# Performance work log

Hardware: AMD Instinct MI355X
Metric: run time of the kernel (lower is better)

Reference implementation:

```python
import jax, jax.numpy as jnp
import numpy as np

N = 50000          # num_nodes
D = 32             # latent_dim
E2 = 800000        # undirected edge pairs; E = 2*E2 directed edges
STEP = 1.0         # step_size


def setup_inputs() -> dict:
    key = jax.random.key(0)
    k1, k2, k3, k4 = jax.random.split(key, 4)
    # Build a symmetric edge list so every edge (s,t) has its reverse (t,s).
    rng = np.random.default_rng(0)
    src = rng.integers(0, N, size=E2)
    dst = rng.integers(0, N, size=E2)
    edge_index = jnp.asarray(
        np.stack([np.concatenate([src, dst]), np.concatenate([dst, src])]),
        dtype=jnp.int32)                                   # [2, 2*E2]
    # reverse-edge index: edge e in first half <-> e+E2 in second half
    right_idx = jnp.asarray(
        np.concatenate([np.arange(E2) + E2, np.arange(E2)]), dtype=jnp.int32)
    x = jax.random.normal(k1, (N, D), dtype=jnp.float32)
    sheaf_W = jax.random.normal(k2, (1, 2 * D), dtype=jnp.float32) * 0.1
    lin_W = jax.random.normal(k3, (D, D), dtype=jnp.float32) * 0.1
    lin_b = jax.random.normal(k4, (D,), dtype=jnp.float32) * 0.1
    return {"x": x, "sheaf_W": sheaf_W, "lin_W": lin_W, "lin_b": lin_b,
            "edge_index": edge_index, "right_idx": right_idx}


def reference(x, sheaf_W, lin_W, lin_b, edge_index, right_idx):
    row, col = edge_index[0], edge_index[1]
    # predict_restriction_maps: maps = tanh(W_s [x_row ; x_col])  -> [E, 1]
    xe = jnp.concatenate([x[row], x[col]], axis=1)          # [E, 2D]
    maps = jnp.tanh(xe @ sheaf_W.T)                         # [E, 1]
    # build_laplacian (left_idx is identity)
    non_diag = -(maps * maps[right_idx])                    # [E, 1]
    diag_maps = jax.ops.segment_sum(maps ** 2, row, num_segments=N)  # [N, 1]
    d_si = (diag_maps + 1.0) ** -0.5                        # [N, 1]
    norm_maps = d_si[row] * non_diag * d_si[col]            # [E, 1]
    diag = (d_si * diag_maps * d_si)[:, 0]                  # [N]
    # y = linear(x); sparse Laplacian matmul: L @ y
    y = x @ lin_W.T + lin_b                                 # [N, D]
    Ly = diag[:, None] * y + jax.ops.segment_sum(
        norm_maps * y[col], row, num_segments=N)            # [N, D]
    return x - STEP * Ly
```

## Files before the change

### kernel.cpp

```cpp
#include <hip/hip_runtime.h>

#define D 32
#define GBITS 6
#define GSIZE 64
#define BLK 256
#define PPC 4096
#define IPT 16
#define CAP 2560

typedef unsigned long long ull;

static __device__ __forceinline__ unsigned short f2h(float f) {
    _Float16 h = (_Float16)f;
    return __builtin_bit_cast(unsigned short, h);
}
static __device__ __forceinline__ float h2f(unsigned short u) {
    return (float)__builtin_bit_cast(_Float16, u);
}
static __device__ __forceinline__ float ftanh(float u) {
    u = fminf(fmaxf(u, -15.f), 15.f);
    float e = __expf(2.f * u);
    return (e - 1.f) / (e + 1.f);
}

__global__ void k_pre_hist(const float* __restrict__ x,
                           const float* __restrict__ sheafW,
                           const float* __restrict__ linW,
                           const float* __restrict__ linb,
                           const int* __restrict__ ei,
                           float2* __restrict__ ab,
                           unsigned short* __restrict__ y_h,
                           int* __restrict__ bhist,
                           int N, int E2, int E, int nbN, int nblkH, int NBG) {
    if (blockIdx.x < nbN) {
        __shared__ float sW[D * D];
        __shared__ float sB[D];
        __shared__ float sS[2 * D];
        for (int i = threadIdx.x; i < D * D; i += blockDim.x) sW[i] = linW[i];
        if (threadIdx.x < D) sB[threadIdx.x] = linb[threadIdx.x];
        if (threadIdx.x < 2 * D) sS[threadIdx.x] = sheafW[threadIdx.x];
        __syncthreads();

        int n = blockIdx.x * blockDim.x + threadIdx.x;
        if (n >= N) return;

        float xv[D];
        const float4* xp = reinterpret_cast<const float4*>(x + (size_t)n * D);
#pragma unroll
        for (int i = 0; i < D / 4; ++i) {
            float4 v = xp[i];
            xv[4 * i + 0] = v.x; xv[4 * i + 1] = v.y;
            xv[4 * i + 2] = v.z; xv[4 * i + 3] = v.w;
        }

        float av = 0.f, bv = 0.f;
#pragma unroll
        for (int d = 0; d < D; ++d) { av += xv[d] * sS[d]; bv += xv[d] * sS[D + d]; }
        ab[n] = make_float2(av, bv);

        unsigned short yh[D];
#pragma unroll
        for (int j = 0; j < D; ++j) {
            float s = sB[j];
#pragma unroll
            for (int d = 0; d < D; ++d) s += xv[d] * sW[j * D + d];
            yh[j] = f2h(s);
        }
        uint4* dst = reinterpret_cast<uint4*>(y_h + (size_t)n * D);
        const uint4* src = reinterpret_cast<const uint4*>(yh);
#pragma unroll
        for (int q = 0; q < D / 8; ++q) dst[q] = src[q];
    } else {
        __shared__ int hist[1024];
        int blk = blockIdx.x - nbN;
        for (int i = threadIdx.x; i < NBG; i += BLK) hist[i] = 0;
        __syncthreads();
        int base = blk * PPC;
#pragma unroll
        for (int k = 0; k < IPT; ++k) {
            int i = base + k * BLK + threadIdx.x;
            if (i < E2) {
                int s = ei[i];
                int t = ei[E + i];
                atomicAdd(&hist[s >> GBITS], 1);
                atomicAdd(&hist[t >> GBITS], 1);
            }
        }
        __syncthreads();
        for (int i = threadIdx.x; i < NBG; i += BLK)
            bhist[(size_t)i * nblkH + blk] = hist[i];
    }
}

__global__ void k_scanA(int* __restrict__ data, int* __restrict__ bsum, int M) {
    __shared__ int s[256];
    int t = threadIdx.x;
    int i = blockIdx.x * 256 + t;
    int v = (i < M) ? data[i] : 0;
    s[t] = v;
    __syncthreads();
#pragma unroll
    for (int o = 1; o < 256; o <<= 1) {
        int tmp = (t >= o) ? s[t - o] : 0;
        __syncthreads();
        s[t] += tmp;
        __syncthreads();
    }
    if (i < M) data[i] = s[t] - v;
    if (t == 255) bsum[blockIdx.x] = s[255];
}

__global__ void k_scanB(int* __restrict__ data, int NB) {
    __shared__ int s[1024];
    int t = threadIdx.x;
    int per = (NB + 1023) >> 10;
    int beg = t * per;
    int end_ = min(beg + per, NB);
    int sum = 0;
    for (int i = beg; i < end_; ++i) sum += data[i];
    s[t] = sum;
    __syncthreads();
#pragma unroll
    for (int o = 1; o < 1024; o <<= 1) {
        int tmp = (t >= o) ? s[t - o] : 0;
        __syncthreads();
        s[t] += tmp;
        __syncthreads();
    }
    int run = s[t] - sum;
    for (int i = beg; i < end_; ++i) { int v = data[i]; data[i] = run; run += v; }
}

__global__ void k_scatter(const int* __restrict__ ei,
                          const float2* __restrict__ ab,
                          const int* __restrict__ bhist,
                          const int* __restrict__ bsum,
                          ull* __restrict__ binned,
                          int E2, int E, int nblkH, int NBG) {
    __shared__ int cursor[1024];
    for (int i = threadIdx.x; i < NBG; i += BLK) {
        int idx = i * nblkH + blockIdx.x;
        cursor[i] = bhist[idx] + bsum[idx >> 8];
    }
    __syncthreads();
    int base = blockIdx.x * PPC;
#pragma unroll
    for (int k = 0; k < IPT; ++k) {
        int i = base + k * BLK + threadIdx.x;
        if (i < E2) {
            int s = ei[i];
            int t = ei[E + i];
            float2 as = ab[s], at = ab[t];
            float m  = ftanh(as.x + at.y);
            float mr = ftanh(at.x + as.y);
            ull hm = f2h(m), hmr = f2h(mr);
            int pos = atomicAdd(&cursor[s >> GBITS], 1);
            binned[pos] = ((ull)(unsigned)s << 48) | ((ull)(unsigned)t << 32) | (hm << 16) | hmr;
            int pos2 = atomicAdd(&cursor[t >> GBITS], 1);
            binned[pos2] = ((ull)(unsigned)t << 48) | ((ull)(unsigned)s << 32) | (hmr << 16) | hm;
        }
    }
}

__global__ void k_diag(const ull* __restrict__ binned,
                       const int* __restrict__ bhist,
                       const int* __restrict__ bsum,
                       float* __restrict__ dsi, float* __restrict__ diag2,
                       int* __restrict__ rbase_g, int* __restrict__ rcnt_g,
                       int E, int nblkH, int NBG, int N) {
    __shared__ float rdiag[GSIZE];
    __shared__ int rhist[GSIZE];
    __shared__ int ss[GSIZE];
    __shared__ int sgs[2];
    int g = blockIdx.x, t = threadIdx.x;
    if (t < GSIZE) { rdiag[t] = 0.f; rhist[t] = 0; }
    if (t < 2) {
        int gg = g + t;
        if (gg < NBG) {
            int idx = gg * nblkH;
            sgs[t] = bhist[idx] + bsum[idx >> 8];
        } else sgs[t] = E;
    }
    __syncthreads();
    int gstart = sgs[0], gend = sgs[1];
    for (int k = gstart + t; k < gend; k += BLK) {
        ull it = binned[k];
        int r = (int)(it >> 48) & (GSIZE - 1);
        float m = h2f((unsigned short)((it >> 16) & 0xFFFF));
        atomicAdd(&rdiag[r], m * m);
        atomicAdd(&rhist[r], 1);
    }
    __syncthreads();
    int v = (t < GSIZE) ? rhist[t] : 0;
    if (t < GSIZE) ss[t] = v;
    __syncthreads();
#pragma unroll
    for (int o = 1; o < GSIZE; o <<= 1) {
        int tmp = 0;
        if (t < GSIZE && t >= o) tmp = ss[t - o];
        __syncthreads();
        if (t < GSIZE) ss[t] += tmp;
        __syncthreads();
    }
    int n0 = g << GBITS;
    if (t < GSIZE) {
        int n = n0 + t;
        if (n < N) {
            float dm = rdiag[t];
            float ds = rsqrtf(dm + 1.0f);
            dsi[n] = ds;
            diag2[n] = dm * ds * ds;
            rbase_g[n] = ss[t] - v;
            rcnt_g[n] = v;
        }
    }
}

__global__ __launch_bounds__(512) void k_gather_fused(
        const ull* __restrict__ binned,
        const int* __restrict__ bhist,
        const int* __restrict__ bsum,
        const unsigned short* __restrict__ y_h,
        const float* __restrict__ x,
        const float* __restrict__ dsi,
        const float* __restrict__ diag2,
        const int* __restrict__ rbase_g,
        const int* __restrict__ rcnt_g,
        float* __restrict__ out,
        int E, int nblkH, int NBG, int N) {
    __shared__ unsigned int sortedw[CAP];
    __shared__ int rbase[GSIZE];
    __shared__ int rcnt[GSIZE];
    __shared__ int cur[GSIZE];
    __shared__ float sds[GSIZE];
    __shared__ float sdg[GSIZE];
    __shared__ int sgs[1];
    int g = blockIdx.x, t = threadIdx.x;
    int n0 = g << GBITS;
    if (t < GSIZE) {
        int n = n0 + t;
        if (n < N) {
            sds[t] = dsi[n]; sdg[t] = diag2[n];
            int rb = rbase_g[n];
            rbase[t] = rb; cur[t] = rb; rcnt[t] = rcnt_g[n];
        } else { rbase[t] = 0; cur[t] = 0; rcnt[t] = 0; }
    }
    if (t == 0) {
        int idx = g * nblkH;
        sgs[0] = bhist[idx] + bsum[idx >> 8];
    }
    __syncthreads();
    int gstart = sgs[0];
    int cnt = 0;
    {
        int lastn = min(n0 + GSIZE, N) - 1;
        if (lastn >= n0) cnt = min(rbase[lastn - n0] + rcnt[lastn - n0], CAP);
    }

    for (int k = t; k < cnt; k += 512) {
        ull it = binned[gstart + k];
        int r = (int)(it >> 48) & (GSIZE - 1);
        unsigned int c = (unsigned int)((it >> 32) & 0xFFFF);
        float w = h2f((unsigned short)((it >> 16) & 0xFFFF)) *
                  h2f((unsigned short)(it & 0xFFFF)) * dsi[c];
        int pos = atomicAdd(&cur[r], 1);
        sortedw[pos] = (c << 16) | (unsigned int)f2h(w);
    }
    __syncthreads();

    int hw = t >> 5;
    int lane = t & 31;
    int rows = min(GSIZE, N - n0);
    for (int r = hw; r < rows; r += 16) {
        int beg = rbase[r];
        int end_ = beg + rcnt[r];
        float acc = 0.f;
        int k = beg;
        for (; k + 4 <= end_; k += 4) {
            unsigned int e0 = sortedw[k + 0];
            unsigned int e1 = sortedw[k + 1];
            unsigned int e2 = sortedw[k + 2];
            unsigned int e3 = sortedw[k + 3];
            float v0 = h2f(y_h[(size_t)(e0 >> 16) * D + lane]);
            float v1 = h2f(y_h[(size_t)(e1 >> 16) * D + lane]);
            float v2 = h2f(y_h[(size_t)(e2 >> 16) * D + lane]);
            float v3 = h2f(y_h[(size_t)(e3 >> 16) * D + lane]);
            acc += h2f((unsigned short)(e0 & 0xFFFF)) * v0;
            acc += h2f((unsigned short)(e1 & 0xFFFF)) * v1;
            acc += h2f((unsigned short)(e2 & 0xFFFF)) * v2;
            acc += h2f((unsigned short)(e3 & 0xFFFF)) * v3;
        }
        for (; k < end_; ++k) {
            unsigned int e = sortedw[k];
            acc += h2f((unsigned short)(e & 0xFFFF)) *
                   h2f(y_h[(size_t)(e >> 16) * D + lane]);
        }
        size_t p = (size_t)(n0 + r) * D + lane;
        float yown = h2f(y_h[p]);
        out[p] = x[p] - sdg[r] * yown + sds[r] * acc;
    }
}

extern "C" void kernel_launch(void* const* d_in, const int* in_sizes, int n_in,
                              void* d_out, int out_size, void* d_ws, size_t ws_size,
                              hipStream_t stream) {
    const float* x      = (const float*)d_in[0];
    const float* sheafW = (const float*)d_in[1];
    const float* linW   = (const float*)d_in[2];
    const float* linb   = (const float*)d_in[3];
    const int*   ei     = (const int*)d_in[4];

    int N  = in_sizes[0] / D;
    int E  = in_sizes[4] / 2;
    int E2 = E / 2;

    int NBG   = (N + GSIZE - 1) >> GBITS;
    int nblkH = (E2 + PPC - 1) / PPC;
    int MH    = NBG * nblkH;
    int nblkA = (MH + 255) / 256;

    char* wp = (char*)d_ws;
    ull*    binned = (ull*)wp;    wp += (size_t)E * 8;
    float2* ab     = (float2*)wp; wp += (size_t)N * 8;
    float*  dsi    = (float*)wp;  wp += (size_t)N * 4;
    float*  diag2  = (float*)wp;  wp += (size_t)N * 4;
    unsigned short* y_h = (unsigned short*)wp; wp += (size_t)N * D * 2;
    int*    bhist  = (int*)wp;    wp += (size_t)MH * 4;
    int*    bsumA  = (int*)wp;    wp += (size_t)nblkA * 4;
    int*    rbase_g= (int*)wp;    wp += (size_t)N * 4;
    int*    rcnt_g = (int*)wp;    wp += (size_t)N * 4;

    float* out = (float*)d_out;

    int nbN = (N + BLK - 1) / BLK;

    k_pre_hist<<<nbN + nblkH, BLK, 0, stream>>>(x, sheafW, linW, linb, ei, ab, y_h,
                                                bhist, N, E2, E, nbN, nblkH, NBG);
    k_scanA<<<nblkA, 256, 0, stream>>>(bhist, bsumA, MH);
    k_scanB<<<1, 1024, 0, stream>>>(bsumA, nblkA);
    k_scatter<<<nblkH, BLK, 0, stream>>>(ei, ab, bhist, bsumA, binned, E2, E, nblkH, NBG);
    k_diag<<<NBG, BLK, 0, stream>>>(binned, bhist, bsumA, dsi, diag2, rbase_g, rcnt_g,
                                    E, nblkH, NBG, N);
    k_gather_fused<<<NBG, 512, 0, stream>>>(binned, bhist, bsumA, y_h, x, dsi, diag2,
                                            rbase_g, rcnt_g, out, E, nblkH, NBG, N);
}
```

Measured before the change: 92.14 us.

## Merge scan, scatter, diag and gather into one cooperative persistent kernel

Replaces five separate launches (two scan passes, scatter, diag, gather) with a single cooperative kernel of 512 blocks that uses grid.sync between phases and grid-stride loops over chunks and node groups. Histogram/scatter partition size is halved so more chunks exist, and the scan block width changes to 512. The aim is to remove kernel launch gaps and tail effects between short dependent stages. In exchange, each phase runs on a fixed grid that may underfill or serialize work, grid-wide barriers have their own cost, and the 512-thread blocks with large shared arrays may limit residency.

```diff
diff --git a/kernel.cpp b/kernel.cpp
--- a/kernel.cpp
+++ b/kernel.cpp
@@ -1,11 +1,17 @@
 #include <hip/hip_runtime.h>
+#include <hip/hip_cooperative_groups.h>
+
+namespace cg = cooperative_groups;
 
 #define D 32
 #define GBITS 6
 #define GSIZE 64
-#define BLK 256
-#define PPC 4096
-#define IPT 16
+#define BLKP 256
+#define PPC 2048
+#define IPT_H 8
+#define CBLK 512
+#define IPT_S 4
+#define GRID 512
 #define CAP 2560
 
 typedef unsigned long long ull;
@@ -73,12 +79,12 @@
     } else {
         __shared__ int hist[1024];
         int blk = blockIdx.x - nbN;
-        for (int i = threadIdx.x; i < NBG; i += BLK) hist[i] = 0;
+        for (int i = threadIdx.x; i < NBG; i += BLKP) hist[i] = 0;
         __syncthreads();
         int base = blk * PPC;
 #pragma unroll
-        for (int k = 0; k < IPT; ++k) {
-            int i = base + k * BLK + threadIdx.x;
+        for (int k = 0; k < IPT_H; ++k) {
+            int i = base + k * BLKP + threadIdx.x;
             if (i < E2) {
                 int s = ei[i];
                 int t = ei[E + i];
@@ -87,217 +93,217 @@
             }
         }
         __syncthreads();
-        for (int i = threadIdx.x; i < NBG; i += BLK)
+        for (int i = threadIdx.x; i < NBG; i += BLKP)
             bhist[(size_t)i * nblkH + blk] = hist[i];
     }
 }
 
-__global__ void k_scanA(int* __restrict__ data, int* __restrict__ bsum, int M) {
-    __shared__ int s[256];
-    int t = threadIdx.x;
-    int i = blockIdx.x * 256 + t;
-    int v = (i < M) ? data[i] : 0;
-    s[t] = v;
-    __syncthreads();
-#pragma unroll
-    for (int o = 1; o < 256; o <<= 1) {
-        int tmp = (t >= o) ? s[t - o] : 0;
-        __syncthreads();
-        s[t] += tmp;
-        __syncthreads();
-    }
-    if (i < M) data[i] = s[t] - v;
-    if (t == 255) bsum[blockIdx.x] = s[255];
-}
-
-__global__ void k_scanB(int* __restrict__ data, int NB) {
-    __shared__ int s[1024];
-    int t = threadIdx.x;
-    int per = (NB + 1023) >> 10;
-    int beg = t * per;
-    int end_ = min(beg + per, NB);
-    int sum = 0;
-    for (int i = beg; i < end_; ++i) sum += data[i];
-    s[t] = sum;
-    __syncthreads();
-#pragma unroll
-    for (int o = 1; o < 1024; o <<= 1) {
-        int tmp = (t >= o) ? s[t - o] : 0;
-        __syncthreads();
-        s[t] += tmp;
-        __syncthreads();
-    }
-    int run = s[t] - sum;
-    for (int i = beg; i < end_; ++i) { int v = data[i]; data[i] = run; run += v; }
-}
-
-__global__ void k_scatter(const int* __restrict__ ei,
-                          const float2* __restrict__ ab,
-                          const int* __restrict__ bhist,
-                          const int* __restrict__ bsum,
-                          ull* __restrict__ binned,
-                          int E2, int E, int nblkH, int NBG) {
+__global__ __launch_bounds__(CBLK, 4) void k_coop(
+        const int* __restrict__ ei,
+        const float2* __restrict__ ab,
+        int* __restrict__ bhist,
+        int* __restrict__ bsum,
+        ull* __restrict__ binned,
+        const unsigned short* __restrict__ y_h,
+        const float* __restrict__ x,
+        float* __restrict__ dsi,
+        float* __restrict__ diag2,
+        int* __restrict__ rbase_g,
+        int* __restrict__ rcnt_g,
+        float* __restrict__ out,
+        int E2, int E, int nblkH, int NBG, int N, int MH, int nchA) {
+    cg::grid_group grid = cg::this_grid();
+    int bid = blockIdx.x, t = threadIdx.x;
+
+    __shared__ int s512[CBLK];
     __shared__ int cursor[1024];
-    for (int i = threadIdx.x; i < NBG; i += BLK) {
-        int idx = i * nblkH + blockIdx.x;
-        cursor[i] = bhist[idx] + bsum[idx >> 8];
-    }
-    __syncthreads();
-    int base = blockIdx.x * PPC;
-#pragma unroll
-    for (int k = 0; k < IPT; ++k) {
-        int i = base + k * BLK + threadIdx.x;
-        if (i < E2) {
-            int s = ei[i];
-            int t = ei[E + i];
-            float2 as = ab[s], at = ab[t];
-            float m  = ftanh(as.x + at.y);
-            float mr = ftanh(at.x + as.y);
-            ull hm = f2h(m), hmr = f2h(mr);
-            int pos = atomicAdd(&cursor[s >> GBITS], 1);
-            binned[pos] = ((ull)(unsigned)s << 48) | ((ull)(unsigned)t << 32) | (hm << 16) | hmr;
-            int pos2 = atomicAdd(&cursor[t >> GBITS], 1);
-            binned[pos2] = ((ull)(unsigned)t << 48) | ((ull)(unsigned)s << 32) | (hmr << 16) | hm;
-        }
-    }
-}
-
-__global__ void k_diag(const ull* __restrict__ binned,
-                       const int* __restrict__ bhist,
-                       const int* __restrict__ bsum,
-                       float* __restrict__ dsi, float* __restrict__ diag2,
-                       int* __restrict__ rbase_g, int* __restrict__ rcnt_g,
-                       int E, int nblkH, int NBG, int N) {
+    __shared__ unsigned int sortedw[CAP];
     __shared__ float rdiag[GSIZE];
     __shared__ int rhist[GSIZE];
     __shared__ int ss[GSIZE];
-    __shared__ int sgs[2];
-    int g = blockIdx.x, t = threadIdx.x;
-    if (t < GSIZE) { rdiag[t] = 0.f; rhist[t] = 0; }
-    if (t < 2) {
-        int gg = g + t;
-        if (gg < NBG) {
-            int idx = gg * nblkH;
-            sgs[t] = bhist[idx] + bsum[idx >> 8];
-        } else sgs[t] = E;
-    }
-    __syncthreads();
-    int gstart = sgs[0], gend = sgs[1];
-    for (int k = gstart + t; k < gend; k += BLK) {
-        ull it = binned[k];
-        int r = (int)(it >> 48) & (GSIZE - 1);
-        float m = h2f((unsigned short)((it >> 16) & 0xFFFF));
-        atomicAdd(&rdiag[r], m * m);
-        atomicAdd(&rhist[r], 1);
-    }
-    __syncthreads();
-    int v = (t < GSIZE) ? rhist[t] : 0;
-    if (t < GSIZE) ss[t] = v;
-    __syncthreads();
-#pragma unroll
-    for (int o = 1; o < GSIZE; o <<= 1) {
-        int tmp = 0;
-        if (t < GSIZE && t >= o) tmp = ss[t - o];
-        __syncthreads();
-        if (t < GSIZE) ss[t] += tmp;
-        __syncthreads();
-    }
-    int n0 = g << GBITS;
-    if (t < GSIZE) {
-        int n = n0 + t;
-        if (n < N) {
-            float dm = rdiag[t];
-            float ds = rsqrtf(dm + 1.0f);
-            dsi[n] = ds;
-            diag2[n] = dm * ds * ds;
-            rbase_g[n] = ss[t] - v;
-            rcnt_g[n] = v;
-        }
-    }
-}
-
-__global__ __launch_bounds__(512) void k_gather_fused(
-        const ull* __restrict__ binned,
-        const int* __restrict__ bhist,
-        const int* __restrict__ bsum,
-        const unsigned short* __restrict__ y_h,
-        const float* __restrict__ x,
-        const float* __restrict__ dsi,
-        const float* __restrict__ diag2,
-        const int* __restrict__ rbase_g,
-        const int* __restrict__ rcnt_g,
-        float* __restrict__ out,
-        int E, int nblkH, int NBG, int N) {
-    __shared__ unsigned int sortedw[CAP];
     __shared__ int rbase[GSIZE];
     __shared__ int rcnt[GSIZE];
     __shared__ int cur[GSIZE];
     __shared__ float sds[GSIZE];
     __shared__ float sdg[GSIZE];
-    __shared__ int sgs[1];
-    int g = blockIdx.x, t = threadIdx.x;
-    int n0 = g << GBITS;
-    if (t < GSIZE) {
-        int n = n0 + t;
-        if (n < N) {
-            sds[t] = dsi[n]; sdg[t] = diag2[n];
-            int rb = rbase_g[n];
-            rbase[t] = rb; cur[t] = rb; rcnt[t] = rcnt_g[n];
-        } else { rbase[t] = 0; cur[t] = 0; rcnt[t] = 0; }
-    }
-    if (t == 0) {
-        int idx = g * nblkH;
-        sgs[0] = bhist[idx] + bsum[idx >> 8];
-    }
-    __syncthreads();
-    int gstart = sgs[0];
-    int cnt = 0;
-    {
-        int lastn = min(n0 + GSIZE, N) - 1;
-        if (lastn >= n0) cnt = min(rbase[lastn - n0] + rcnt[lastn - n0], CAP);
-    }
-
-    for (int k = t; k < cnt; k += 512) {
-        ull it = binned[gstart + k];
-        int r = (int)(it >> 48) & (GSIZE - 1);
-        unsigned int c = (unsigned int)((it >> 32) & 0xFFFF);
-        float w = h2f((unsigned short)((it >> 16) & 0xFFFF)) *
-                  h2f((unsigned short)(it & 0xFFFF)) * dsi[c];
-        int pos = atomicAdd(&cur[r], 1);
-        sortedw[pos] = (c << 16) | (unsigned int)f2h(w);
-    }
-    __syncthreads();
-
-    int hw = t >> 5;
-    int lane = t & 31;
-    int rows = min(GSIZE, N - n0);
-    for (int r = hw; r < rows; r += 16) {
-        int beg = rbase[r];
-        int end_ = beg + rcnt[r];
-        float acc = 0.f;
-        int k = beg;
-        for (; k + 4 <= end_; k += 4) {
-            unsigned int e0 = sortedw[k + 0];
-            unsigned int e1 = sortedw[k + 1];
-            unsigned int e2 = sortedw[k + 2];
-            unsigned int e3 = sortedw[k + 3];
-            float v0 = h2f(y_h[(size_t)(e0 >> 16) * D + lane]);
-            float v1 = h2f(y_h[(size_t)(e1 >> 16) * D + lane]);
-            float v2 = h2f(y_h[(size_t)(e2 >> 16) * D + lane]);
-            float v3 = h2f(y_h[(size_t)(e3 >> 16) * D + lane]);
-            acc += h2f((unsigned short)(e0 & 0xFFFF)) * v0;
-            acc += h2f((unsigned short)(e1 & 0xFFFF)) * v1;
-            acc += h2f((unsigned short)(e2 & 0xFFFF)) * v2;
-            acc += h2f((unsigned short)(e3 & 0xFFFF)) * v3;
-        }
-        for (; k < end_; ++k) {
-            unsigned int e = sortedw[k];
-            acc += h2f((unsigned short)(e & 0xFFFF)) *
-                   h2f(y_h[(size_t)(e >> 16) * D + lane]);
-        }
-        size_t p = (size_t)(n0 + r) * D + lane;
-        float yown = h2f(y_h[p]);
-        out[p] = x[p] - sdg[r] * yown + sds[r] * acc;
+    __shared__ int sgs[2];
+
+    for (int c = bid; c < nchA; c += GRID) {
+        int i = c * CBLK + t;
+        int v = (i < MH) ? bhist[i] : 0;
+        s512[t] = v;
+        __syncthreads();
+#pragma unroll
+        for (int o = 1; o < CBLK; o <<= 1) {
+            int tmp = (t >= o) ? s512[t - o] : 0;
+            __syncthreads();
+            s512[t] += tmp;
+            __syncthreads();
+        }
+        if (i < MH) bhist[i] = s512[t] - v;
+        if (t == CBLK - 1) bsum[c] = s512[t];
+        __syncthreads();
+    }
+    grid.sync();
+
+    if (bid == 0) {
+        int per = (nchA + CBLK - 1) / CBLK;
+        int beg = t * per;
+        int end_ = min(beg + per, nchA);
+        int sum = 0;
+        for (int i = beg; i < end_; ++i) sum += bsum[i];
+        s512[t] = sum;
+        __syncthreads();
+#pragma unroll
+        for (int o = 1; o < CBLK; o <<= 1) {
+            int tmp = (t >= o) ? s512[t - o] : 0;
+            __syncthreads();
+            s512[t] += tmp;
+            __syncthreads();
+        }
+        int run = s512[t] - sum;
+        for (int i = beg; i < end_; ++i) { int v = bsum[i]; bsum[i] = run; run += v; }
+    }
+    grid.sync();
+
+    for (int c = bid; c < nblkH; c += GRID) {
+        for (int i = t; i < NBG; i += CBLK) {
+            int idx = i * nblkH + c;
+            cursor[i] = bhist[idx] + bsum[idx >> 9];
+        }
+        __syncthreads();
+        int base = c * PPC;
+#pragma unroll
+        for (int k = 0; k < IPT_S; ++k) {
+            int i = base + k * CBLK + t;
+            if (i < E2) {
+                int s = ei[i];
+                int tt = ei[E + i];
+                float2 as = ab[s], at = ab[tt];
+                float m  = ftanh(as.x + at.y);
+                float mr = ftanh(at.x + as.y);
+                ull hm = f2h(m), hmr = f2h(mr);
+                int pos = atomicAdd(&cursor[s >> GBITS], 1);
+                binned[pos] = ((ull)(unsigned)s << 48) | ((ull)(unsigned)tt << 32) | (hm << 16) | hmr;
+                int pos2 = atomicAdd(&cursor[tt >> GBITS], 1);
+                binned[pos2] = ((ull)(unsigned)tt << 48) | ((ull)(unsigned)s << 32) | (hmr << 16) | hm;
+            }
+        }
+        __syncthreads();
+    }
+    grid.sync();
+
+    for (int g = bid; g < NBG; g += GRID) {
+        if (t < GSIZE) { rdiag[t] = 0.f; rhist[t] = 0; }
+        if (t < 2) {
+            int gg = g + t;
+            if (gg < NBG) {
+                int idx = gg * nblkH;
+                sgs[t] = bhist[idx] + bsum[idx >> 9];
+            } else sgs[t] = E;
+        }
+        __syncthreads();
+        int gstart = sgs[0], gend = sgs[1];
+        for (int k = gstart + t; k < gend; k += CBLK) {
+            ull it = binned[k];
+            int r = (int)(it >> 48) & (GSIZE - 1);
+            float m = h2f((unsigned short)((it >> 16) & 0xFFFF));
+            atomicAdd(&rdiag[r], m * m);
+            atomicAdd(&rhist[r], 1);
+        }
+        __syncthreads();
+        int v = (t < GSIZE) ? rhist[t] : 0;
+        if (t < GSIZE) ss[t] = v;
+        __syncthreads();
+#pragma unroll
+        for (int o = 1; o < GSIZE; o <<= 1) {
+            int tmp = 0;
+            if (t < GSIZE && t >= o) tmp = ss[t - o];
+            __syncthreads();
+            if (t < GSIZE) ss[t] += tmp;
+            __syncthreads();
+        }
+        int n0 = g << GBITS;
+        if (t < GSIZE) {
+            int n = n0 + t;
+            if (n < N) {
+                float dm = rdiag[t];
+                float ds = rsqrtf(dm + 1.0f);
+                dsi[n] = ds;
+                diag2[n] = dm * ds * ds;
+                rbase_g[n] = ss[t] - v;
+                rcnt_g[n] = v;
+            }
+        }
+        __syncthreads();
+    }
+    grid.sync();
+
+    for (int g = bid; g < NBG; g += GRID) {
+        int n0 = g << GBITS;
+        if (t < GSIZE) {
+            int n = n0 + t;
+            if (n < N) {
+                sds[t] = dsi[n]; sdg[t] = diag2[n];
+                int rb = rbase_g[n];
+                rbase[t] = rb; cur[t] = rb; rcnt[t] = rcnt_g[n];
+            } else { rbase[t] = 0; cur[t] = 0; rcnt[t] = 0; }
+        }
+        if (t == 0) {
+            int idx = g * nblkH;
+            sgs[0] = bhist[idx] + bsum[idx >> 9];
+        }
+        __syncthreads();
+        int gstart = sgs[0];
+        int cnt = 0;
+        {
+            int lastn = min(n0 + GSIZE, N) - 1;
+            if (lastn >= n0) cnt = min(rbase[lastn - n0] + rcnt[lastn - n0], CAP);
+        }
+
+        for (int k = t; k < cnt; k += CBLK) {
+            ull it = binned[gstart + k];
+            int r = (int)(it >> 48) & (GSIZE - 1);
+            unsigned int c = (unsigned int)((it >> 32) & 0xFFFF);
+            float w = h2f((unsigned short)((it >> 16) & 0xFFFF)) *
+                      h2f((unsigned short)(it & 0xFFFF)) * dsi[c];
+            int pos = atomicAdd(&cur[r], 1);
+            sortedw[pos] = (c << 16) | (unsigned int)f2h(w);
+        }
+        __syncthreads();
+
+        int hw = t >> 5;
+        int lane = t & 31;
+        int rows = min(GSIZE, N - n0);
+        for (int r = hw; r < rows; r += 16) {
+            int beg = rbase[r];
+            int end_ = beg + rcnt[r];
+            float acc = 0.f;
+            int k = beg;
+            for (; k + 4 <= end_; k += 4) {
+                unsigned int e0 = sortedw[k + 0];
+                unsigned int e1 = sortedw[k + 1];
+                unsigned int e2 = sortedw[k + 2];
+                unsigned int e3 = sortedw[k + 3];
+                float v0 = h2f(y_h[(size_t)(e0 >> 16) * D + lane]);
+                float v1 = h2f(y_h[(size_t)(e1 >> 16) * D + lane]);
+                float v2 = h2f(y_h[(size_t)(e2 >> 16) * D + lane]);
+                float v3 = h2f(y_h[(size_t)(e3 >> 16) * D + lane]);
+                acc += h2f((unsigned short)(e0 & 0xFFFF)) * v0;
+                acc += h2f((unsigned short)(e1 & 0xFFFF)) * v1;
+                acc += h2f((unsigned short)(e2 & 0xFFFF)) * v2;
+                acc += h2f((unsigned short)(e3 & 0xFFFF)) * v3;
+            }
+            for (; k < end_; ++k) {
+                unsigned int e = sortedw[k];
+                acc += h2f((unsigned short)(e & 0xFFFF)) *
+                       h2f(y_h[(size_t)(e >> 16) * D + lane]);
+            }
+            size_t p = (size_t)(n0 + r) * D + lane;
+            float yown = h2f(y_h[p]);
+            out[p] = x[p] - sdg[r] * yown + sds[r] * acc;
+        }
+        __syncthreads();
     }
 }
 
@@ -317,7 +323,7 @@
     int NBG   = (N + GSIZE - 1) >> GBITS;
     int nblkH = (E2 + PPC - 1) / PPC;
     int MH    = NBG * nblkH;
-    int nblkA = (MH + 255) / 256;
+    int nchA  = (MH + CBLK - 1) / CBLK;
 
     char* wp = (char*)d_ws;
     ull*    binned = (ull*)wp;    wp += (size_t)E * 8;
@@ -326,21 +332,22 @@
     float*  diag2  = (float*)wp;  wp += (size_t)N * 4;
     unsigned short* y_h = (unsigned short*)wp; wp += (size_t)N * D * 2;
     int*    bhist  = (int*)wp;    wp += (size_t)MH * 4;
-    int*    bsumA  = (int*)wp;    wp += (size_t)nblkA * 4;
+    int*    bsum   = (int*)wp;    wp += (size_t)nchA * 4;
     int*    rbase_g= (int*)wp;    wp += (size_t)N * 4;
     int*    rcnt_g = (int*)wp;    wp += (size_t)N * 4;
 
     float* out = (float*)d_out;
 
-    int nbN = (N + BLK - 1) / BLK;
-
-    k_pre_hist<<<nbN + nblkH, BLK, 0, stream>>>(x, sheafW, linW, linb, ei, ab, y_h,
-                                                bhist, N, E2, E, nbN, nblkH, NBG);
-    k_scanA<<<nblkA, 256, 0, stream>>>(bhist, bsumA, MH);
-    k_scanB<<<1, 1024, 0, stream>>>(bsumA, nblkA);
-    k_scatter<<<nblkH, BLK, 0, stream>>>(ei, ab, bhist, bsumA, binned, E2, E, nblkH, NBG);
-    k_diag<<<NBG, BLK, 0, stream>>>(binned, bhist, bsumA, dsi, diag2, rbase_g, rcnt_g,
-                                    E, nblkH, NBG, N);
-    k_gather_fused<<<NBG, 512, 0, stream>>>(binned, bhist, bsumA, y_h, x, dsi, diag2,
-                                            rbase_g, rcnt_g, out, E, nblkH, NBG, N);
-}
+    int nbN = (N + BLKP - 1) / BLKP;
+
+    k_pre_hist<<<nbN + nblkH, BLKP, 0, stream>>>(x, sheafW, linW, linb, ei, ab, y_h,
+                                                 bhist, N, E2, E, nbN, nblkH, NBG);
+
+    void* args[] = { (void*)&ei, (void*)&ab, (void*)&bhist, (void*)&bsum,
+                     (void*)&binned, (void*)&y_h, (void*)&x, (void*)&dsi,
+                     (void*)&diag2, (void*)&rbase_g, (void*)&rcnt_g, (void*)&out,
+                     (void*)&E2, (void*)&E, (void*)&nblkH, (void*)&NBG,
+                     (void*)&N, (void*)&MH, (void*)&nchA };
+    hipLaunchCooperativeKernel((const void*)k_coop, dim3(GRID), dim3(CBLK),
+                               args, 0, stream);
+}
```

New measurement: 321.9 us. +249.3%, slower.
